# Kernel tuning notes

Hardware: AMD Instinct MI355X
Metric: run time of the kernel (lower is better)

## Reference

```python
import jax, jax.numpy as jnp
import numpy as np

# Module hyperparameters (from init_kwargs)
HID = 2048          # hidden_dim
LAT = 512           # kv_latent_dim
H = 16              # num_heads
D = HID // H        # head_dim = 128
FORGET_P = 0.1      # forget_prob
WIN = 128           # window_size
SINK = 16           # persistent_tokens
B, S = 2, 2048
NEG = -1e9


def setup_inputs() -> dict:
    key = jax.random.key(0)
    ks = jax.random.split(key, 8)
    scale = 0.02
    x = jax.random.normal(ks[0], (B, S, HID), dtype=jnp.float32)
    W_q = jax.random.normal(ks[1], (HID, HID), dtype=jnp.float32) * scale
    W_dkv = jax.random.normal(ks[2], (HID, LAT), dtype=jnp.float32) * scale
    W_uk = jax.random.normal(ks[3], (LAT, HID), dtype=jnp.float32) * scale
    W_uv = jax.random.normal(ks[4], (LAT, HID), dtype=jnp.float32) * scale
    W_o = jax.random.normal(ks[5], (HID, HID), dtype=jnp.float32) * scale
    # Bernoulli(forget_prob) per-key forget mask (1 = forget this token)
    forget_mask = jax.random.bernoulli(ks[6], FORGET_P, (B, S)).astype(jnp.int32)
    return {"x": x, "W_q": W_q, "W_dkv": W_dkv, "W_uk": W_uk,
            "W_uv": W_uv, "W_o": W_o, "forget_mask": forget_mask, "top_k": 64}


def reference(x, W_q, W_dkv, W_uk, W_uv, W_o, forget_mask, top_k):
    Bx, Sx, _ = x.shape
    # Queries; keys/values via shared compressed KV latent (MLA-style)
    q = (x @ W_q).reshape(Bx, Sx, H, D)
    c = x @ W_dkv                                   # [B, S, LAT]
    k = (c @ W_uk).reshape(Bx, Sx, H, D)
    v = (c @ W_uv).reshape(Bx, Sx, H, D)

    scores = jnp.einsum('bqhd,bkhd->bhqk', q, k) / np.float32(np.sqrt(D))

    qi = jnp.arange(Sx)[:, None]
    ki = jnp.arange(Sx)[None, :]
    causal = ki <= qi
    local = ki >= qi - (WIN - 1)
    sink = ki < SINK                  # persistent sink tokens always visible
    allow = causal & (local | sink)   # [S, S]

    # Forgetting: drop non-sink, non-self keys flagged by the forget mask
    forget = (forget_mask[:, None, None, :] == 1) \
             & (ki >= SINK)[None, None] & (ki != qi)[None, None]   # [B,1,S,S]
    keep = allow[None, None] & ~forget

    s = jnp.where(keep, scores, jnp.asarray(NEG, scores.dtype))
    # Top-k selection per query: keep only the k largest scores
    kth = jax.lax.top_k(s, top_k)[0][..., -1:]
    s = jnp.where(s >= kth, s, jnp.asarray(NEG, s.dtype))

    attn = jax.nn.softmax(s, axis=-1)
    out = jnp.einsum('bhqk,bkhd->bqhd', attn, v).reshape(Bx, Sx, HID)
    return out @ W_o
```

## Files before the change

kernel.cpp:

```cpp
#include <hip/hip_runtime.h>
#include <hip/hip_bf16.h>

typedef unsigned short u16;
typedef unsigned int u32;
typedef unsigned long long u64;
typedef __bf16 bf16x8 __attribute__((ext_vector_type(8)));
typedef float f32x4 __attribute__((ext_vector_type(4)));
typedef u16 u16x4 __attribute__((ext_vector_type(4)));
typedef u16 u16x8 __attribute__((ext_vector_type(8)));

static constexpr int BB = 2, SS = 2048, HIDC = 2048, LATC = 512, NH = 16, HD = 128;
static constexpr int MROWS = BB * SS;
static constexpr float NEGV = -1e9f;

__device__ __forceinline__ u16 f2bf(float f) {
  __hip_bfloat16 h = __float2bfloat16(f);
  return __builtin_bit_cast(u16, h);
}
__device__ __forceinline__ float bf2f(u16 u) {
  return __uint_as_float(((u32)u) << 16);
}
__device__ __forceinline__ void load_lds16(const void* g, void* l) {
  __builtin_amdgcn_global_load_lds(
      (const __attribute__((address_space(1))) void*)g,
      (__attribute__((address_space(3))) void*)l, 16, 0, 0);
}

template <int MODE>
__global__ __launch_bounds__(256, 2) void gemm_bt(
    const u16* __restrict__ A, const u16* __restrict__ Bt,
    float* __restrict__ C, u16* __restrict__ Cb, int M, int N, int K) {
  __shared__ u16 As[128 * 64];
  __shared__ u16 Bs[128 * 64];
  const int tid = threadIdx.x;
  const int lane = tid & 63;
  const int wv = tid >> 6;
  const int wr = wv >> 1, wc = wv & 1;
  const int m0 = blockIdx.x * 128, n0 = blockIdx.y * 128;

  f32x4 acc[4][4];
#pragma unroll
  for (int i = 0; i < 4; ++i)
#pragma unroll
    for (int j = 0; j < 4; ++j) acc[i][j] = (f32x4){0.f, 0.f, 0.f, 0.f};

  int srow[4], sgc[4];
#pragma unroll
  for (int j = 0; j < 4; ++j) {
    int e = j * 2048 + tid * 8;
    int row = e >> 6;
    int slot = (e >> 3) & 7;
    srow[j] = row;
    sgc[j] = (slot ^ (row & 7)) * 8;
  }

  for (int k0 = 0; k0 < K; k0 += 64) {
    __syncthreads();
#pragma unroll
    for (int j = 0; j < 4; ++j) {
      const u16* ga = A + (size_t)(m0 + srow[j]) * K + k0 + sgc[j];
      const u16* gb = Bt + (size_t)(n0 + srow[j]) * K + k0 + sgc[j];
      load_lds16(ga, &As[j * 2048 + wv * 512]);
      load_lds16(gb, &Bs[j * 2048 + wv * 512]);
    }
    asm volatile("s_waitcnt vmcnt(0)" ::: "memory");
    __syncthreads();

#pragma unroll
    for (int kk = 0; kk < 2; ++kk) {
      bf16x8 afr[4], bfr[4];
      const int kg = kk * 4 + (lane >> 4);
#pragma unroll
      for (int i = 0; i < 4; ++i) {
        int ar = wr * 64 + i * 16 + (lane & 15);
        afr[i] = *(const bf16x8*)&As[ar * 64 + ((kg ^ (ar & 7)) << 3)];
        int br = wc * 64 + i * 16 + (lane & 15);
        bfr[i] = *(const bf16x8*)&Bs[br * 64 + ((kg ^ (br & 7)) << 3)];
      }
#pragma unroll
      for (int mi = 0; mi < 4; ++mi)
#pragma unroll
        for (int ni = 0; ni < 4; ++ni)
          acc[mi][ni] = __builtin_amdgcn_mfma_f32_16x16x32_bf16(
              afr[mi], bfr[ni], acc[mi][ni], 0, 0, 0);
    }
  }

#pragma unroll
  for (int mi = 0; mi < 4; ++mi) {
#pragma unroll
    for (int ni = 0; ni < 4; ++ni) {
      const int row = m0 + wr * 64 + mi * 16 + (lane >> 4) * 4;
      const int col = n0 + wc * 64 + ni * 16 + (lane & 15);
#pragma unroll
      for (int r = 0; r < 4; ++r) {
        size_t off = (size_t)(row + r) * N + col;
        if constexpr (MODE == 0) C[off] = acc[mi][ni][r];
        if constexpr (MODE == 2) Cb[off] = f2bf(acc[mi][ni][r]);
      }
    }
  }
}

template <int TN, int MODE>
__global__ __launch_bounds__(256, 2) void gemm_split_bt(
    const u16* __restrict__ Ah, const u16* __restrict__ Al,
    const u16* __restrict__ Bth, const u16* __restrict__ Btl,
    float* __restrict__ C, u16* __restrict__ Ch, u16* __restrict__ Cl,
    int M, int N, int K) {
  constexpr int NI = TN / 32;
  __shared__ u16 Ash[128 * 64];
  __shared__ u16 Asl[128 * 64];
  __shared__ u16 Bsh[TN * 64];
  __shared__ u16 Bsl[TN * 64];
  const int tid = threadIdx.x;
  const int lane = tid & 63;
  const int wv = tid >> 6;
  const int wr = wv >> 1, wc = wv & 1;
  const int l15 = lane & 15, lhi = lane >> 4;
  const int m0 = blockIdx.x * 128, n0 = blockIdx.y * TN;

  f32x4 acc[4][NI];
#pragma unroll
  for (int i = 0; i < 4; ++i)
#pragma unroll
    for (int j = 0; j < NI; ++j) acc[i][j] = (f32x4){0.f, 0.f, 0.f, 0.f};

  int srow[4], sgc[4];
#pragma unroll
  for (int j = 0; j < 4; ++j) {
    int e = j * 2048 + tid * 8;
    int row = e >> 6;
    int slot = (e >> 3) & 7;
    srow[j] = row;
    sgc[j] = (slot ^ (row & 7)) * 8;
  }

  for (int k0 = 0; k0 < K; k0 += 64) {
    __syncthreads();
#pragma unroll
    for (int j = 0; j < 4; ++j) {
      const size_t ao = (size_t)(m0 + srow[j]) * K + k0 + sgc[j];
      load_lds16(Ah + ao, &Ash[j * 2048 + wv * 512]);
      load_lds16(Al + ao, &Asl[j * 2048 + wv * 512]);
    }
#pragma unroll
    for (int j = 0; j < NI; ++j) {
      const size_t bo = (size_t)(n0 + srow[j]) * K + k0 + sgc[j];
      load_lds16(Bth + bo, &Bsh[j * 2048 + wv * 512]);
      load_lds16(Btl + bo, &Bsl[j * 2048 + wv * 512]);
    }
    asm volatile("s_waitcnt vmcnt(0)" ::: "memory");
    __syncthreads();

#pragma unroll
    for (int kk = 0; kk < 2; ++kk) {
      const int kg = kk * 4 + lhi;
      bf16x8 afh[4], afl[4], bfh[NI], bfl[NI];
#pragma unroll
      for (int i = 0; i < 4; ++i) {
        const int ar = wr * 64 + i * 16 + l15;
        const int off = ar * 64 + ((kg ^ (ar & 7)) << 3);
        afh[i] = *(const bf16x8*)&Ash[off];
        afl[i] = *(const bf16x8*)&Asl[off];
      }
#pragma unroll
      for (int i = 0; i < NI; ++i) {
        const int br = wc * (TN / 2) + i * 16 + l15;
        const int off = br * 64 + ((kg ^ (br & 7)) << 3);
        bfh[i] = *(const bf16x8*)&Bsh[off];
        bfl[i] = *(const bf16x8*)&Bsl[off];
      }
#pragma unroll
      for (int mi = 0; mi < 4; ++mi)
#pragma unroll
        for (int ni = 0; ni < NI; ++ni) {
          acc[mi][ni] = __builtin_amdgcn_mfma_f32_16x16x32_bf16(
              afh[mi], bfh[ni], acc[mi][ni], 0, 0, 0);
          acc[mi][ni] = __builtin_amdgcn_mfma_f32_16x16x32_bf16(
              afh[mi], bfl[ni], acc[mi][ni], 0, 0, 0);
          acc[mi][ni] = __builtin_amdgcn_mfma_f32_16x16x32_bf16(
              afl[mi], bfh[ni], acc[mi][ni], 0, 0, 0);
        }
    }
  }

#pragma unroll
  for (int mi = 0; mi < 4; ++mi) {
#pragma unroll
    for (int ni = 0; ni < NI; ++ni) {
      const int row = m0 + wr * 64 + mi * 16 + lhi * 4;
      const int col = n0 + wc * (TN / 2) + ni * 16 + l15;
#pragma unroll
      for (int r = 0; r < 4; ++r) {
        const size_t off = (size_t)(row + r) * N + col;
        const float v = acc[mi][ni][r];
        if constexpr (MODE == 0) C[off] = v;
        if constexpr (MODE == 3) {
          const u16 hh = f2bf(v);
          Ch[off] = hh;
          Cl[off] = f2bf(v - bf2f(hh));
        }
      }
    }
  }
}

__global__ __launch_bounds__(1024) void transpose_split(
    const float* __restrict__ W, u16* __restrict__ Th, u16* __restrict__ Tl,
    int K, int N) {
  __shared__ float t[32][33];
  const int tx = threadIdx.x, ty = threadIdx.y;
  t[ty][tx] = W[(size_t)(blockIdx.y * 32 + ty) * N + blockIdx.x * 32 + tx];
  __syncthreads();
  const float v = t[tx][ty];
  const u16 hi = f2bf(v);
  const u16 lo = f2bf(v - bf2f(hi));
  const size_t o = (size_t)(blockIdx.x * 32 + ty) * K + blockIdx.y * 32 + tx;
  Th[o] = hi;
  Tl[o] = lo;
}

__global__ __launch_bounds__(1024) void transpose_one(
    const float* __restrict__ W, u16* __restrict__ T, int K, int N) {
  __shared__ float t[32][33];
  const int tx = threadIdx.x, ty = threadIdx.y;
  t[ty][tx] = W[(size_t)(blockIdx.y * 32 + ty) * N + blockIdx.x * 32 + tx];
  __syncthreads();
  const size_t o = (size_t)(blockIdx.x * 32 + ty) * K + blockIdx.y * 32 + tx;
  T[o] = f2bf(t[tx][ty]);
}

__global__ void split_ew(const float* __restrict__ in, u16* __restrict__ hi,
                         u16* __restrict__ lo, int n) {
  const size_t i = ((size_t)blockIdx.x * blockDim.x + threadIdx.x) * 4;
  if (i >= (size_t)n) return;
  f32x4 v = *(const f32x4*)(in + i);
  u16x4 h, l;
#pragma unroll
  for (int e = 0; e < 4; ++e) {
    float f = v[e];
    u16 hh = f2bf(f);
    h[e] = hh;
    l[e] = f2bf(f - bf2f(hh));
  }
  *(u16x4*)(hi + i) = h;
  *(u16x4*)(lo + i) = l;
}

__device__ __forceinline__ u32 fmap(float f) {
  u32 b = __float_as_uint(f);
  return (b & 0x80000000u) ? ~b : (b | 0x80000000u);
}
__device__ __forceinline__ float unfmap(u32 u) {
  return (u & 0x80000000u) ? __uint_as_float(u ^ 0x80000000u)
                           : __uint_as_float(~u);
}

__global__ __launch_bounds__(512, 2) void attn_v6(
    const u16* __restrict__ qbh, const u16* __restrict__ qbl,
    const u16* __restrict__ khi, const u16* __restrict__ klo,
    const u16* __restrict__ vt, const int* __restrict__ forget,
    const int* __restrict__ topk, u16* __restrict__ ab) {
  __shared__ u16 KP[2 * 64 * 128];
  __shared__ float St[64 * 68];
  __shared__ u16 Vb1[64 * 128];
  __shared__ int fm[256];
  u16* const Kh = KP;
  u16* const Kl = KP + 64 * 128;
  u16* const Pb = KP;
  u16* const Vt0 = (u16*)St;

  const float scale = 0.08838834764831845f;
  const int tid = threadIdx.x, lane = tid & 63, wv = tid >> 6;
  const int lin = blockIdx.x + 32 * (blockIdx.y + 16 * blockIdx.z);
  const int nl = (lin & 7) * 128 + (lin >> 3);
  const int q0 = (nl & 31) * 64;
  const int h = (nl >> 5) & 15;
  const int b = nl >> 9;
  const int mt = wv >> 1, nh = wv & 1;
  const int l15 = lane & 15, lhi = lane >> 4;
  const int nt = (q0 >= 256) ? 4 : (q0 / 64 + 1);
  const int KTOP = topk[0];

  auto kbase = [&](int t) {
    return (q0 >= 256) ? (t == 0 ? 0 : q0 + t * 64 - 192) : t * 64;
  };
  auto stage_k = [&](int t) {
    const int kbt = kbase(t);
#pragma unroll
    for (int p = 0; p < 2; ++p) {
      const int c = p * 512 + tid;
      const int row = c >> 4, sl = c & 15;
      const size_t src = (size_t)(b * SS + kbt + row) * HIDC + h * HD +
                         ((sl ^ (row & 7)) << 3);
      load_lds16(khi + src, Kh + (p * 512 + wv * 64) * 8);
      load_lds16(klo + src, Kl + (p * 512 + wv * 64) * 8);
    }
  };
  auto stage_vt = [&](int t, u16* dst) {
    const int kbt = kbase(t);
#pragma unroll
    for (int p = 0; p < 2; ++p) {
      const int c = p * 512 + tid;
      const int d = c >> 3, sl = c & 7;
      const u16* src = vt + ((size_t)(b * HIDC + h * HD + d)) * SS + kbt +
                       ((sl ^ (d & 7)) << 3);
      load_lds16(src, dst + (p * 512 + wv * 64) * 8);
    }
  };

  if (tid < 256)
    fm[tid] = ((tid >> 6) < nt) ? forget[b * SS + kbase(tid >> 6) + (tid & 63)] : 0;

  u32 koff[4][2];
#pragma unroll
  for (int kt = 0; kt < 4; ++kt)
#pragma unroll
    for (int ni = 0; ni < 2; ++ni) {
      const int key = nh * 32 + ni * 16 + l15;
      const int kg = kt * 4 + lhi;
      koff[kt][ni] = key * 128 + ((kg ^ (key & 7)) << 3);
    }
  const int arow = mt * 16 + l15;
  u32 pboff[2];
#pragma unroll
  for (int ks = 0; ks < 2; ++ks)
    pboff[ks] = arow * 256 + (((ks * 4 + lhi) ^ (arow & 7)) << 3);
  u32 voff[2][4];
#pragma unroll
  for (int ks = 0; ks < 2; ++ks)
#pragma unroll
    for (int t2 = 0; t2 < 4; ++t2) {
      const int drow = nh * 64 + t2 * 16 + l15;
      voff[ks][t2] = drow * 64 + (((ks * 4 + lhi) ^ (drow & 7)) << 3);
    }
  const u32 stw = (u32)(mt * 16 + lhi * 4) * 68 + nh * 32 + l15;

  u16x8 ah[4], al[4];
  const size_t qrow = (size_t)(b * SS + q0 + mt * 16 + l15) * HIDC + h * HD;
#pragma unroll
  for (int kt = 0; kt < 4; ++kt) {
    ah[kt] = *(const u16x8*)(qbh + qrow + kt * 32 + lhi * 8);
    al[kt] = *(const u16x8*)(qbl + qrow + kt * 32 + lhi * 8);
  }

  u32 uu[8][4];
#pragma unroll
  for (int i = 0; i < 8; ++i)
#pragma unroll
    for (int j = 0; j < 4; ++j) uu[i][j] = 0u;

  stage_k(0);
#pragma unroll
  for (int t = 0; t < 4; ++t) {
    if (t < nt) {
      asm volatile("s_waitcnt vmcnt(0)" ::: "memory");
      __syncthreads();

      f32x4 acc0 = (f32x4){0.f, 0.f, 0.f, 0.f};
      f32x4 acc1 = (f32x4){0.f, 0.f, 0.f, 0.f};
#pragma unroll
      for (int kt = 0; kt < 4; ++kt) {
#pragma unroll
        for (int ni = 0; ni < 2; ++ni) {
          const bf16x8 bh = *(const bf16x8*)(Kh + koff[kt][ni]);
          const bf16x8 bl = *(const bf16x8*)(Kl + koff[kt][ni]);
          f32x4 a = ni ? acc1 : acc0;
          a = __builtin_amdgcn_mfma_f32_16x16x32_bf16(
              __builtin_bit_cast(bf16x8, ah[kt]), bh, a, 0, 0, 0);
          a = __builtin_amdgcn_mfma_f32_16x16x32_bf16(
              __builtin_bit_cast(bf16x8, ah[kt]), bl, a, 0, 0, 0);
          a = __builtin_amdgcn_mfma_f32_16x16x32_bf16(
              __builtin_bit_cast(bf16x8, al[kt]), bh, a, 0, 0, 0);
          if (ni) acc1 = a; else acc0 = a;
        }
      }
#pragma unroll
      for (int ni = 0; ni < 2; ++ni)
#pragma unroll
        for (int r = 0; r < 4; ++r)
          St[stw + r * 68 + ni * 16] = (ni ? acc1 : acc0)[r] * scale;
      __syncthreads();

      if (t + 1 < nt) stage_k(t + 1);

      const int kbt = kbase(t);
      const int key = kbt + lane;
      const bool fok = !(fm[t * 64 + lane] != 0 && key >= 16);
      const bool sk = key < 16;
#pragma unroll
      for (int i = 0; i < 8; ++i) {
        const int qi = q0 + wv * 8 + i;
        const bool valid =
            key <= qi && (key >= qi - 127 || sk) && (fok || key == qi);
        uu[i][t] = fmap(valid ? St[(wv * 8 + i) * 68 + lane] : NEGV);
      }
    }
  }
  __syncthreads();

  stage_vt(0, Vt0);

  u32 tl[8], th[8];
#pragma unroll
  for (int i = 0; i < 8; ++i) { tl[i] = 0u; th[i] = 0xFFFFFFFFu; }
  for (int it = 0; it < 32; ++it) {
    bool any = false;
#pragma unroll
    for (int i = 0; i < 8; ++i) {
      if (tl[i] < th[i]) {
        any = true;
        const u32 mid = tl[i] + ((th[i] - tl[i]) >> 1) + 1u;
        const int cnt = __popcll(__ballot(uu[i][0] >= mid)) +
                        __popcll(__ballot(uu[i][1] >= mid)) +
                        __popcll(__ballot(uu[i][2] >= mid)) +
                        __popcll(__ballot(uu[i][3] >= mid));
        if (cnt == KTOP) {
          tl[i] = mid;
          th[i] = mid;
        } else if (cnt > KTOP) {
          tl[i] = mid;
        } else {
          th[i] = mid - 1u;
        }
      }
    }
    if (!any) break;
  }

#pragma unroll
  for (int i = 0; i < 8; ++i) {
    const int r = wv * 8 + i;
    float sv[4], m = NEGV;
#pragma unroll
    for (int j = 0; j < 4; ++j) {
      sv[j] = unfmap(uu[i][j]);
      m = (uu[i][j] >= tl[i]) ? fmaxf(m, sv[j]) : m;
    }
#pragma unroll
    for (int off = 32; off > 0; off >>= 1) m = fmaxf(m, __shfl_xor(m, off));
    float e[4], z = 0.f;
#pragma unroll
    for (int j = 0; j < 4; ++j) {
      e[j] = (uu[i][j] >= tl[i]) ? __expf(sv[j] - m) : 0.f;
      z += e[j];
    }
#pragma unroll
    for (int off = 32; off > 0; off >>= 1) z += __shfl_xor(z, off);
    const float rz = 1.f / z;
#pragma unroll
    for (int j = 0; j < 4; ++j) {
      const int c = lane + 64 * j;
      const int sl = c >> 3;
      Pb[r * 256 + ((sl ^ (r & 7)) << 3) + (c & 7)] = f2bf(e[j] * rz);
    }
  }

  asm volatile("s_waitcnt vmcnt(0)" ::: "memory");
  __syncthreads();

  f32x4 pacc[4];
#pragma unroll
  for (int t2 = 0; t2 < 4; ++t2) pacc[t2] = (f32x4){0.f, 0.f, 0.f, 0.f};

#pragma unroll
  for (int t = 0; t < 4; ++t) {
    if (t < nt) {
      if (t + 1 < nt) stage_vt(t + 1, ((t + 1) & 1) ? Vb1 : Vt0);
      const u16* Vcur = (t & 1) ? Vb1 : Vt0;
#pragma unroll
      for (int ks = 0; ks < 2; ++ks) {
        const bf16x8 af = *(const bf16x8*)(Pb + pboff[ks] + t * 64);
#pragma unroll
        for (int t2 = 0; t2 < 4; ++t2) {
          const bf16x8 bf_ = *(const bf16x8*)(Vcur + voff[ks][t2]);
          pacc[t2] = __builtin_amdgcn_mfma_f32_16x16x32_bf16(af, bf_, pacc[t2],
                                                             0, 0, 0);
        }
      }
      if (t + 1 < nt) {
        asm volatile("s_waitcnt vmcnt(0)" ::: "memory");
        __syncthreads();
      }
    }
  }

#pragma unroll
  for (int t2 = 0; t2 < 4; ++t2)
#pragma unroll
    for (int r = 0; r < 4; ++r) {
      const int row = q0 + mt * 16 + lhi * 4 + r;
      const int col = h * HD + nh * 64 + t2 * 16 + l15;
      ab[(size_t)(b * SS + row) * HIDC + col] = f2bf(pacc[t2][r]);
    }
}

extern "C" void kernel_launch(void* const* d_in, const int* in_sizes, int n_in,
                              void* d_out, int out_size, void* d_ws, size_t ws_size,
                              hipStream_t stream) {
  const float* x = (const float*)d_in[0];
  const float* W_q = (const float*)d_in[1];
  const float* W_dkv = (const float*)d_in[2];
  const float* W_uk = (const float*)d_in[3];
  const float* W_uv = (const float*)d_in[4];
  const float* W_o = (const float*)d_in[5];
  const int* forget = (const int*)d_in[6];
  const int* topk = (const int*)d_in[7];
  float* out = (float*)d_out;

  char* p = (char*)d_ws;
  auto take = [&](size_t n) {
    char* r = p;
    p += (n + 255) & ~(size_t)255;
    return r;
  };

  u16* xb_hi = (u16*)take((size_t)MROWS * HIDC * 2);
  u16* xb_lo = (u16*)take((size_t)MROWS * HIDC * 2);
  u16* Wqh = (u16*)take((size_t)HIDC * HIDC * 2);
  u16* Wql = (u16*)take((size_t)HIDC * HIDC * 2);
  u16* Wdh = (u16*)take((size_t)LATC * HIDC * 2);
  u16* Wdl = (u16*)take((size_t)LATC * HIDC * 2);
  u16* Wukh = (u16*)take((size_t)HIDC * LATC * 2);
  u16* Wukl = (u16*)take((size_t)HIDC * LATC * 2);
  u16* Wuvt = (u16*)take((size_t)HIDC * LATC * 2);
  u16* Wot = (u16*)take((size_t)HIDC * HIDC * 2);
  u16* qbh = (u16*)take((size_t)MROWS * HIDC * 2);
  u16* qbl = (u16*)take((size_t)MROWS * HIDC * 2);
  u16* cbh = (u16*)take((size_t)MROWS * LATC * 2);
  u16* cbl = (u16*)take((size_t)MROWS * LATC * 2);
  u16* vt = (u16*)take((size_t)BB * HIDC * SS * 2);
  u16* khi = xb_hi;
  u16* klo = xb_lo;
  u16* ab = Wqh;

  const dim3 tb(32, 32);
  split_ew<<<dim3((MROWS * HIDC / 4) / 256), dim3(256), 0, stream>>>(
      x, xb_hi, xb_lo, MROWS * HIDC);
  transpose_split<<<dim3(HIDC / 32, HIDC / 32), tb, 0, stream>>>(W_q, Wqh, Wql, HIDC, HIDC);
  transpose_split<<<dim3(LATC / 32, HIDC / 32), tb, 0, stream>>>(W_dkv, Wdh, Wdl, HIDC, LATC);
  transpose_split<<<dim3(HIDC / 32, LATC / 32), tb, 0, stream>>>(W_uk, Wukh, Wukl, LATC, HIDC);
  transpose_one<<<dim3(HIDC / 32, LATC / 32), tb, 0, stream>>>(W_uv, Wuvt, LATC, HIDC);
  transpose_one<<<dim3(HIDC / 32, HIDC / 32), tb, 0, stream>>>(W_o, Wot, HIDC, HIDC);

  gemm_split_bt<128, 3><<<dim3(MROWS / 128, HIDC / 128), 256, 0, stream>>>(
      xb_hi, xb_lo, Wqh, Wql, nullptr, qbh, qbl, MROWS, HIDC, HIDC);
  gemm_split_bt<64, 3><<<dim3(MROWS / 128, LATC / 64), 256, 0, stream>>>(
      xb_hi, xb_lo, Wdh, Wdl, nullptr, cbh, cbl, MROWS, LATC, HIDC);
  gemm_split_bt<128, 3><<<dim3(MROWS / 128, HIDC / 128), 256, 0, stream>>>(
      cbh, cbl, Wukh, Wukl, nullptr, khi, klo, MROWS, HIDC, LATC);
  const dim3 gv(HIDC / 128, SS / 128);
  gemm_bt<2><<<gv, 256, 0, stream>>>(Wuvt, cbh, nullptr, vt, HIDC, SS, LATC);
  gemm_bt<2><<<gv, 256, 0, stream>>>(Wuvt, cbh + (size_t)SS * LATC, nullptr,
                                     vt + (size_t)HIDC * SS, HIDC, SS, LATC);
  attn_v6<<<dim3(SS / 64, NH, BB), dim3(512), 0, stream>>>(
      qbh, qbl, khi, klo, vt, forget, topk, ab);
  gemm_bt<0><<<dim3(MROWS / 128, HIDC / 128), 256, 0, stream>>>(
      ab, Wot, out, nullptr, MROWS, HIDC, HIDC);
}
```

Measured before the change: 330.6 us.

## Fuse prep kernels, batch V GEMM over grid z, and remap blocks across XCDs

Merges the elementwise split of x and the five weight transposes into one prep_all kernel dispatched by block-index range, using 256-thread blocks that each handle four rows. The two per-batch V up-projection GEMMs become a single launch that uses blockIdx.z with strides. Both GEMM kernels gain an XCD-aware block remap so neighbouring tiles land on the same chiplet and share its L2. This cuts launch count and aims to improve cache locality, at the cost of branchy prep logic. The remap assumes the block count is divisible by 8.

```diff
diff --git a/kernel.cpp b/kernel.cpp
--- a/kernel.cpp
+++ b/kernel.cpp
@@ -25,18 +25,33 @@
       (const __attribute__((address_space(1))) void*)g,
       (__attribute__((address_space(3))) void*)l, 16, 0, 0);
 }
+__device__ __forceinline__ void xcd_remap(int& bx, int& by) {
+  const int nbx = gridDim.x;
+  const int nb = nbx * gridDim.y;
+  int lin = blockIdx.x + nbx * blockIdx.y;
+  lin = (lin & 7) * (nb >> 3) + (lin >> 3);
+  bx = lin % nbx;
+  by = lin / nbx;
+}
 
 template <int MODE>
 __global__ __launch_bounds__(256, 2) void gemm_bt(
     const u16* __restrict__ A, const u16* __restrict__ Bt,
-    float* __restrict__ C, u16* __restrict__ Cb, int M, int N, int K) {
+    float* __restrict__ C, u16* __restrict__ Cb, int M, int N, int K,
+    size_t sA, size_t sB, size_t sC) {
   __shared__ u16 As[128 * 64];
   __shared__ u16 Bs[128 * 64];
   const int tid = threadIdx.x;
   const int lane = tid & 63;
   const int wv = tid >> 6;
   const int wr = wv >> 1, wc = wv & 1;
-  const int m0 = blockIdx.x * 128, n0 = blockIdx.y * 128;
+  int bx, by;
+  xcd_remap(bx, by);
+  const int m0 = bx * 128, n0 = by * 128;
+  A += sA * blockIdx.z;
+  Bt += sB * blockIdx.z;
+  if constexpr (MODE == 0) C += sC * blockIdx.z;
+  if constexpr (MODE == 2) Cb += sC * blockIdx.z;
 
   f32x4 acc[4][4];
 #pragma unroll
@@ -118,7 +133,9 @@
   const int wv = tid >> 6;
   const int wr = wv >> 1, wc = wv & 1;
   const int l15 = lane & 15, lhi = lane >> 4;
-  const int m0 = blockIdx.x * 128, n0 = blockIdx.y * TN;
+  int bx, by;
+  xcd_remap(bx, by);
+  const int m0 = bx * 128, n0 = by * TN;
 
   f32x4 acc[4][NI];
 #pragma unroll
@@ -206,46 +223,64 @@
   }
 }
 
-__global__ __launch_bounds__(1024) void transpose_split(
-    const float* __restrict__ W, u16* __restrict__ Th, u16* __restrict__ Tl,
-    int K, int N) {
+__global__ __launch_bounds__(256) void prep_all(
+    const float* __restrict__ x, u16* __restrict__ xh, u16* __restrict__ xl,
+    const float* __restrict__ Wq, u16* __restrict__ Wqh, u16* __restrict__ Wql,
+    const float* __restrict__ Wdkv, u16* __restrict__ Wdh, u16* __restrict__ Wdl,
+    const float* __restrict__ Wuk, u16* __restrict__ Wukh, u16* __restrict__ Wukl,
+    const float* __restrict__ Wuv, u16* __restrict__ Wuvt,
+    const float* __restrict__ Wo, u16* __restrict__ Wot) {
+  const int bx = blockIdx.x, tid = threadIdx.x;
+  if (bx < 8192) {
+    const size_t i = ((size_t)bx * 256 + tid) * 4;
+    f32x4 v = *(const f32x4*)(x + i);
+    u16x4 hh, ll;
+#pragma unroll
+    for (int e = 0; e < 4; ++e) {
+      const u16 hi = f2bf(v[e]);
+      hh[e] = hi;
+      ll[e] = f2bf(v[e] - bf2f(hi));
+    }
+    *(u16x4*)(xh + i) = hh;
+    *(u16x4*)(xl + i) = ll;
+    return;
+  }
   __shared__ float t[32][33];
-  const int tx = threadIdx.x, ty = threadIdx.y;
-  t[ty][tx] = W[(size_t)(blockIdx.y * 32 + ty) * N + blockIdx.x * 32 + tx];
+  const float* W;
+  u16 *Th, *Tl = nullptr;
+  int K, N, gx, gy;
+  if (bx < 12288) {
+    const int q = bx - 8192;
+    W = Wq; Th = Wqh; Tl = Wql; K = 2048; N = 2048; gx = q & 63; gy = q >> 6;
+  } else if (bx < 13312) {
+    const int q = bx - 12288;
+    W = Wdkv; Th = Wdh; Tl = Wdl; K = 2048; N = 512; gx = q & 15; gy = q >> 4;
+  } else if (bx < 14336) {
+    const int q = bx - 13312;
+    W = Wuk; Th = Wukh; Tl = Wukl; K = 512; N = 2048; gx = q & 63; gy = q >> 6;
+  } else if (bx < 15360) {
+    const int q = bx - 14336;
+    W = Wuv; Th = Wuvt; K = 512; N = 2048; gx = q & 63; gy = q >> 6;
+  } else {
+    const int q = bx - 15360;
+    W = Wo; Th = Wot; K = 2048; N = 2048; gx = q & 63; gy = q >> 6;
+  }
+  const int tx = tid & 31, ty0 = tid >> 5;
+#pragma unroll
+  for (int i = 0; i < 4; ++i) {
+    const int ty = ty0 + i * 8;
+    t[ty][tx] = W[(size_t)(gy * 32 + ty) * N + gx * 32 + tx];
+  }
   __syncthreads();
-  const float v = t[tx][ty];
-  const u16 hi = f2bf(v);
-  const u16 lo = f2bf(v - bf2f(hi));
-  const size_t o = (size_t)(blockIdx.x * 32 + ty) * K + blockIdx.y * 32 + tx;
-  Th[o] = hi;
-  Tl[o] = lo;
-}
-
-__global__ __launch_bounds__(1024) void transpose_one(
-    const float* __restrict__ W, u16* __restrict__ T, int K, int N) {
-  __shared__ float t[32][33];
-  const int tx = threadIdx.x, ty = threadIdx.y;
-  t[ty][tx] = W[(size_t)(blockIdx.y * 32 + ty) * N + blockIdx.x * 32 + tx];
-  __syncthreads();
-  const size_t o = (size_t)(blockIdx.x * 32 + ty) * K + blockIdx.y * 32 + tx;
-  T[o] = f2bf(t[tx][ty]);
-}
-
-__global__ void split_ew(const float* __restrict__ in, u16* __restrict__ hi,
-                         u16* __restrict__ lo, int n) {
-  const size_t i = ((size_t)blockIdx.x * blockDim.x + threadIdx.x) * 4;
-  if (i >= (size_t)n) return;
-  f32x4 v = *(const f32x4*)(in + i);
-  u16x4 h, l;
-#pragma unroll
-  for (int e = 0; e < 4; ++e) {
-    float f = v[e];
-    u16 hh = f2bf(f);
-    h[e] = hh;
-    l[e] = f2bf(f - bf2f(hh));
-  }
-  *(u16x4*)(hi + i) = h;
-  *(u16x4*)(lo + i) = l;
+#pragma unroll
+  for (int i = 0; i < 4; ++i) {
+    const int ty = ty0 + i * 8;
+    const float v = t[tx][ty];
+    const size_t o = (size_t)(gx * 32 + ty) * K + gy * 32 + tx;
+    const u16 hi = f2bf(v);
+    Th[o] = hi;
+    if (Tl) Tl[o] = f2bf(v - bf2f(hi));
+  }
 }
 
 __device__ __forceinline__ u32 fmap(float f) {
@@ -535,14 +570,9 @@
   u16* klo = xb_lo;
   u16* ab = Wqh;
 
-  const dim3 tb(32, 32);
-  split_ew<<<dim3((MROWS * HIDC / 4) / 256), dim3(256), 0, stream>>>(
-      x, xb_hi, xb_lo, MROWS * HIDC);
-  transpose_split<<<dim3(HIDC / 32, HIDC / 32), tb, 0, stream>>>(W_q, Wqh, Wql, HIDC, HIDC);
-  transpose_split<<<dim3(LATC / 32, HIDC / 32), tb, 0, stream>>>(W_dkv, Wdh, Wdl, HIDC, LATC);
-  transpose_split<<<dim3(HIDC / 32, LATC / 32), tb, 0, stream>>>(W_uk, Wukh, Wukl, LATC, HIDC);
-  transpose_one<<<dim3(HIDC / 32, LATC / 32), tb, 0, stream>>>(W_uv, Wuvt, LATC, HIDC);
-  transpose_one<<<dim3(HIDC / 32, HIDC / 32), tb, 0, stream>>>(W_o, Wot, HIDC, HIDC);
+  prep_all<<<dim3(19456), dim3(256), 0, stream>>>(
+      x, xb_hi, xb_lo, W_q, Wqh, Wql, W_dkv, Wdh, Wdl, W_uk, Wukh, Wukl,
+      W_uv, Wuvt, W_o, Wot);
 
   gemm_split_bt<128, 3><<<dim3(MROWS / 128, HIDC / 128), 256, 0, stream>>>(
       xb_hi, xb_lo, Wqh, Wql, nullptr, qbh, qbl, MROWS, HIDC, HIDC);
@@ -550,12 +580,11 @@
       xb_hi, xb_lo, Wdh, Wdl, nullptr, cbh, cbl, MROWS, LATC, HIDC);
   gemm_split_bt<128, 3><<<dim3(MROWS / 128, HIDC / 128), 256, 0, stream>>>(
       cbh, cbl, Wukh, Wukl, nullptr, khi, klo, MROWS, HIDC, LATC);
-  const dim3 gv(HIDC / 128, SS / 128);
-  gemm_bt<2><<<gv, 256, 0, stream>>>(Wuvt, cbh, nullptr, vt, HIDC, SS, LATC);
-  gemm_bt<2><<<gv, 256, 0, stream>>>(Wuvt, cbh + (size_t)SS * LATC, nullptr,
-                                     vt + (size_t)HIDC * SS, HIDC, SS, LATC);
+  gemm_bt<2><<<dim3(HIDC / 128, SS / 128, BB), 256, 0, stream>>>(
+      Wuvt, cbh, nullptr, vt, HIDC, SS, LATC,
+      0, (size_t)SS * LATC, (size_t)HIDC * SS);
   attn_v6<<<dim3(SS / 64, NH, BB), dim3(512), 0, stream>>>(
       qbh, qbl, khi, klo, vt, forget, topk, ab);
   gemm_bt<0><<<dim3(MROWS / 128, HIDC / 128), 256, 0, stream>>>(
-      ab, Wot, out, nullptr, MROWS, HIDC, HIDC);
-}
+      ab, Wot, out, nullptr, MROWS, HIDC, HIDC, 0, 0, 0);
+}
```

New measurement: 327.8 us. No clear change (-0.8%).
